# Performance work log

Hardware: AMD Instinct MI355X
Metric: run time of the kernel (lower is better)

The kernel has to match this reference:

```python
import jax, jax.numpy as jnp
import numpy as np

B, T, C, H = 4, 2048, 768, 12
D = C // H  # head_size = 64
ROPE_BASE = 10000.0


def rotary_tables(seq_len, dim, dtype=jnp.float32):
    # dim = head_size; uses dim//2 frequencies
    inv_freq = 1.0 / (ROPE_BASE ** (jnp.arange(0, dim, 2, dtype=jnp.float32) / dim))
    t = jnp.arange(seq_len, dtype=jnp.float32)
    freqs = jnp.outer(t, inv_freq)  # [T, D/2]
    return jnp.cos(freqs).astype(dtype), jnp.sin(freqs).astype(dtype)


def apply_rotary(x, cos, sin):
    # x: [B, H, T, D]; cos/sin: [T, D/2] broadcast over B,H
    d = x.shape[-1] // 2
    x1, x2 = x[..., :d], x[..., d:]
    y1 = x1 * cos + x2 * sin
    y2 = -x1 * sin + x2 * cos
    return jnp.concatenate([y1, y2], axis=-1)


def setup_inputs() -> dict:
    key = jax.random.key(0)
    ks = jax.random.split(key, 5)
    x = jax.random.normal(ks[0], (B, T, C), dtype=jnp.float32)
    W_attn = jax.random.normal(ks[1], (C, 3 * C), dtype=jnp.float32) * (1.0 / np.sqrt(C))
    b_attn = jax.random.normal(ks[2], (3 * C,), dtype=jnp.float32) * 0.02
    W_proj = jax.random.normal(ks[3], (C, C), dtype=jnp.float32) * (1.0 / np.sqrt(C))
    b_proj = jax.random.normal(ks[4], (C,), dtype=jnp.float32) * 0.02
    return {"x": x, "W_attn": W_attn, "b_attn": b_attn, "W_proj": W_proj, "b_proj": b_proj}


def reference(x, W_attn, b_attn, W_proj, b_proj):
    Bx, Tx, Cx = x.shape
    qkv = x @ W_attn + b_attn  # [B, T, 3C]
    q, k, v = jnp.split(qkv, 3, axis=-1)
    # [B, T, C] -> [B, H, T, D]
    to_heads = lambda a: a.reshape(Bx, Tx, H, D).transpose(0, 2, 1, 3)
    q, k, v = to_heads(q), to_heads(k), to_heads(v)
    cos, sin = rotary_tables(Tx, D, x.dtype)
    q = apply_rotary(q, cos, sin)
    k = apply_rotary(k, cos, sin)
    scale = 1.0 / np.sqrt(D)
    scores = jnp.einsum('bhqd,bhkd->bhqk', q, k) * scale  # [B, H, T, T]
    causal = jnp.tril(jnp.ones((Tx, Tx), dtype=bool))
    scores = jnp.where(causal, scores, jnp.finfo(scores.dtype).min)
    attn = jax.nn.softmax(scores, axis=-1)
    y = jnp.einsum('bhqk,bhkd->bhqd', attn, v)  # [B, H, T, D]
    y = y.transpose(0, 2, 1, 3).reshape(Bx, Tx, Cx)
    return y @ W_proj + b_proj
```

## Files before the change

### kernel.cpp

```cpp
#include <hip/hip_runtime.h>
#include <hip/hip_bf16.h>

#define BB 4
#define TT 2048
#define CC 768
#define HH 12
#define DD 64
#define MM (BB * TT)
#define BH (BB * HH)

typedef __bf16 bf16_t;
typedef __bf16 bf16x8 __attribute__((ext_vector_type(8)));
typedef __bf16 bf16x4 __attribute__((ext_vector_type(4)));
typedef float f32x4 __attribute__((ext_vector_type(4)));
typedef float f32x16 __attribute__((ext_vector_type(16)));

__device__ __forceinline__ float fast_exp2(float x) {
#if __has_builtin(__builtin_amdgcn_exp2f)
    return __builtin_amdgcn_exp2f(x);
#else
    return exp2f(x);
#endif
}

__device__ __forceinline__ uint32_t pk2(float lo, float hi) {
    bf16_t l = (bf16_t)lo, h = (bf16_t)hi;
    uint16_t lu = __builtin_bit_cast(uint16_t, l);
    uint16_t hu = __builtin_bit_cast(uint16_t, h);
    return ((uint32_t)hu << 16) | lu;
}

__device__ __forceinline__ void gload_lds16(const void* g, void* l) {
    __builtin_amdgcn_global_load_lds(
        (const __attribute__((address_space(1))) uint32_t*)g,
        (__attribute__((address_space(3))) uint32_t*)l, 16, 0, 0);
}

__global__ void cvt_f32_bf16(const float* __restrict__ in, bf16_t* __restrict__ out, int n4) {
    int tid = blockIdx.x * blockDim.x + threadIdx.x;
    if (tid >= n4) return;
    float4 v = ((const float4*)in)[tid];
    bf16x4 o;
    o[0] = (bf16_t)v.x; o[1] = (bf16_t)v.y; o[2] = (bf16_t)v.z; o[3] = (bf16_t)v.w;
    ((bf16x4*)out)[tid] = o;
}

__global__ void transpose_cvt(const float* __restrict__ W, bf16_t* __restrict__ WT, int K, int N) {
    __shared__ bf16_t tile[32][33];
    int k0 = blockIdx.x * 32, n0 = blockIdx.y * 32;
    int tx = threadIdx.x, ty = threadIdx.y;
#pragma unroll
    for (int r = 0; r < 4; ++r) {
        int kl = ty * 4 + r;
        tile[kl][tx] = (bf16_t)W[(size_t)(k0 + kl) * N + n0 + tx];
    }
    __syncthreads();
#pragma unroll
    for (int r = 0; r < 4; ++r) {
        int nl = ty * 4 + r;
        WT[(size_t)(n0 + nl) * K + k0 + tx] = tile[tx][nl];
    }
}

#define GEMM_CORE(A_, BT_, acc_)                                                       \
    __shared__ bf16_t As[2][128 * 32];                                                 \
    __shared__ bf16_t Bs[2][128 * 32];                                                 \
    int tid = threadIdx.x;                                                             \
    int wv = tid >> 6, lane = tid & 63, c = lane & 15, quad = lane >> 4;               \
    int wm = (wv >> 1) * 64, wn = (wv & 1) * 64;                                       \
    int m0 = blockIdx.x * 128, n0 = blockIdx.y * 128;                                  \
    int srow = wv * 32 + (lane >> 2);                                                  \
    int slot = lane & 3;                                                               \
    auto stage = [&](int buf, int k0) {                                                \
        _Pragma("unroll")                                                              \
        for (int ins = 0; ins < 2; ++ins) {                                            \
            int r = srow + ins * 16;                                                   \
            int g = (slot - ((r >> 1) & 3)) & 3;                                       \
            const bf16_t* ga = A_ + (size_t)(m0 + r) * K + k0 + g * 8;                 \
            const bf16_t* gb = BT_ + (size_t)(n0 + r) * K + k0 + g * 8;                \
            gload_lds16(ga, &As[buf][(wv * 32 + ins * 16) * 32]);                      \
            gload_lds16(gb, &Bs[buf][(wv * 32 + ins * 16) * 32]);                      \
        }                                                                              \
    };                                                                                 \
    int s_rd = (quad + ((c >> 1) & 3)) & 3;                                            \
    const int nk = K / 32;                                                             \
    stage(0, 0);                                                                       \
    for (int kt = 0; kt < nk; ++kt) {                                                  \
        __syncthreads();                                                               \
        if (kt + 1 < nk) stage((kt + 1) & 1, (kt + 1) * 32);                           \
        int buf = kt & 1;                                                              \
        bf16x8 af[4], bfr[4];                                                          \
        _Pragma("unroll")                                                              \
        for (int i = 0; i < 4; ++i) af[i] = *(const bf16x8*)&As[buf][(wm + i * 16 + c) * 32 + s_rd * 8];  \
        _Pragma("unroll")                                                              \
        for (int j = 0; j < 4; ++j) bfr[j] = *(const bf16x8*)&Bs[buf][(wn + j * 16 + c) * 32 + s_rd * 8]; \
        _Pragma("unroll")                                                              \
        for (int i = 0; i < 4; ++i)                                                    \
            _Pragma("unroll")                                                          \
            for (int j = 0; j < 4; ++j)                                                \
                acc_[i][j] = __builtin_amdgcn_mfma_f32_16x16x32_bf16(af[i], bfr[j], acc_[i][j], 0, 0, 0); \
    }

__global__ __launch_bounds__(256, 3) void gemm_qkv(
        const bf16_t* __restrict__ A, const bf16_t* __restrict__ BT,
        const float* __restrict__ bias,
        bf16_t* __restrict__ Qh, bf16_t* __restrict__ Kh, bf16_t* __restrict__ Vt) {
    const int K = 768;
    __shared__ __align__(16) bf16_t smem[17408];
    bf16_t* Asp = smem;
    bf16_t* Bsp = smem + 8192;
    int tid = threadIdx.x;
    int wv = tid >> 6, lane = tid & 63, c = lane & 15, quad = lane >> 4;
    int wm = (wv >> 1) * 64, wn = (wv & 1) * 64;
    int m0 = blockIdx.x * 128, n0 = blockIdx.y * 128;
    int srow = wv * 32 + (lane >> 2);
    int slot = lane & 3;
    auto stage = [&](int buf, int k0) {
#pragma unroll
        for (int ins = 0; ins < 2; ++ins) {
            int r = srow + ins * 16;
            int g = (slot - ((r >> 1) & 3)) & 3;
            gload_lds16(A + (size_t)(m0 + r) * K + k0 + g * 8, &Asp[buf * 4096 + (wv * 32 + ins * 16) * 32]);
            gload_lds16(BT + (size_t)(n0 + r) * K + k0 + g * 8, &Bsp[buf * 4096 + (wv * 32 + ins * 16) * 32]);
        }
    };
    int s_rd = (quad + ((c >> 1) & 3)) & 3;
    f32x4 acc[4][4] = {};
    const int nk = K / 32;
    stage(0, 0);
    for (int kt = 0; kt < nk; ++kt) {
        __syncthreads();
        if (kt + 1 < nk) stage((kt + 1) & 1, (kt + 1) * 32);
        int buf = kt & 1;
        bf16x8 af[4], bfr[4];
#pragma unroll
        for (int i = 0; i < 4; ++i) af[i] = *(const bf16x8*)&Asp[buf * 4096 + (wm + i * 16 + c) * 32 + s_rd * 8];
#pragma unroll
        for (int j = 0; j < 4; ++j) bfr[j] = *(const bf16x8*)&Bsp[buf * 4096 + (wn + j * 16 + c) * 32 + s_rd * 8];
#pragma unroll
        for (int i = 0; i < 4; ++i)
#pragma unroll
            for (int j = 0; j < 4; ++j)
                acc[i][j] = __builtin_amdgcn_mfma_f32_16x16x32_bf16(af[i], bfr[j], acc[i][j], 0, 0, 0);
    }
    __syncthreads();

    int type = n0 / 768;
    int hloc = ((n0 % 768) + wn) >> 6;
    int bidx = m0 >> 11;
    int colb = n0 + wn;
    int tb = (m0 + wm) & (TT - 1);
    bf16_t* epi = smem + wv * 4352;
    int rrow = lane >> 3, cchunk = lane & 7;

    if (type < 2) {
        const float rscale = (type == 0) ? 0.125f * 1.44269504088896f : 1.0f;
#pragma unroll
        for (int j = 0; j < 2; ++j) {
            int dlo = j * 16 + c;
            float infr = fast_exp2(-(float)dlo * 0.4152410118609828f);
            float blo = bias[colb + j * 16 + c];
            float bhi = bias[colb + (j + 2) * 16 + c];
#pragma unroll
            for (int i = 0; i < 4; ++i)
#pragma unroll
                for (int r = 0; r < 4; ++r) {
                    int lr = i * 16 + quad * 4 + r;
                    float a = acc[i][j][r] + blo;
                    float b2 = acc[i][j + 2][r] + bhi;
                    float fr = (float)(tb + lr) * infr;
                    float cs, sn;
                    __sincosf(fr, &sn, &cs);
                    epi[lr * 68 + dlo]      = (bf16_t)((a * cs + b2 * sn) * rscale);
                    epi[lr * 68 + dlo + 32] = (bf16_t)((-a * sn + b2 * cs) * rscale);
                }
        }
        bf16_t* dst = (type == 0 ? Qh : Kh) + (size_t)(bidx * HH + hloc) * TT * DD + (size_t)tb * DD;
#pragma unroll
        for (int it = 0; it < 8; ++it) {
            int row = it * 8 + rrow;
            bf16x8 v = *(const bf16x8*)&epi[row * 68 + cchunk * 8];
            *(bf16x8*)&dst[row * 64 + cchunk * 8] = v;
        }
    } else {
        int kt64 = tb >> 6;
#pragma unroll
        for (int j = 0; j < 4; ++j) {
            int dim = j * 16 + c;
            float bv = bias[colb + j * 16 + c];
            int rot = (dim & 7) * 8;
#pragma unroll
            for (int i = 0; i < 4; ++i)
#pragma unroll
                for (int r = 0; r < 4; ++r) {
                    int tin = i * 16 + quad * 4 + r;
                    epi[dim * 68 + ((tin + rot) & 63)] = (bf16_t)(acc[i][j][r] + bv);
                }
        }
        bf16_t* dstV = Vt + (size_t)(bidx * HH + hloc) * (TT / 64) * 4096 + (size_t)kt64 * 4096;
#pragma unroll
        for (int it = 0; it < 8; ++it) {
            int dim = it * 8 + rrow;
            int src = ((cchunk + (dim & 7)) & 7) * 8;
            bf16x8 v = *(const bf16x8*)&epi[dim * 68 + src];
            *(bf16x8*)&dstV[dim * 64 + cchunk * 8] = v;
        }
    }
}

__global__ __launch_bounds__(256, 3) void gemm_proj(
        const bf16_t* __restrict__ A, const bf16_t* __restrict__ BT,
        const float* __restrict__ bias, float* __restrict__ Cout) {
    const int K = 768;
    f32x4 acc[4][4] = {};
    GEMM_CORE(A, BT, acc)
#pragma unroll
    for (int j = 0; j < 4; ++j) {
        int col = n0 + wn + j * 16 + c;
        float bv = bias[col];
#pragma unroll
        for (int i = 0; i < 4; ++i) {
            int row = m0 + wm + i * 16 + quad * 4;
#pragma unroll
            for (int r = 0; r < 4; ++r)
                Cout[(size_t)(row + r) * CC + col] = acc[i][j][r] + bv;
        }
    }
}

__global__ __launch_bounds__(256, 3) void flash_attn(
        const bf16_t* __restrict__ Q, const bf16_t* __restrict__ Kc,
        const bf16_t* __restrict__ Vt, bf16_t* __restrict__ Y) {
    __shared__ bf16_t Ks[2][64 * 64];
    __shared__ bf16_t Vs[2][64 * 64];
    int blk = blockIdx.x;
    int r0 = (blk < 256) ? blk : ((blk < 512) ? (1023 - blk) : (blk - 256));
    int qt = 15 - (r0 / 48);
    int bh = r0 % 48;
    int wv = threadIdx.x >> 6, lane = threadIdx.x & 63;
    int b = bh / HH, h = bh - b * HH;
    int q31 = lane & 31, hi = lane >> 5;
    int qbw = qt * 128 + wv * 32;
    const bf16_t* Qg = Q + ((size_t)bh * TT + qbw) * DD;
    const bf16_t* Kg = Kc + (size_t)bh * TT * DD;
    const bf16_t* Vg = Vt + (size_t)bh * (TT / 64) * 4096;

    bf16x8 qf[4];
#pragma unroll
    for (int dk = 0; dk < 4; ++dk)
        qf[dk] = *(const bf16x8*)(Qg + (size_t)q31 * DD + dk * 16 + hi * 8);

    int srow = wv * 16 + (lane >> 3);
    int slot = lane & 7;
    auto stage = [&](int buf, int kt64) {
#pragma unroll
        for (int ins = 0; ins < 2; ++ins) {
            int r = srow + ins * 8;
            int g = (slot - (r & 7)) & 7;
            gload_lds16(Kg + (size_t)(kt64 * 64 + r) * 64 + g * 8, &Ks[buf][(wv * 16 + ins * 8) * 64]);
            gload_lds16(Vg + (size_t)kt64 * 4096 + r * 64 + g * 8, &Vs[buf][(wv * 16 + ins * 8) * 64]);
        }
    };

    f32x16 O[2] = {};
    float lsum = 0.0f;

    int ntiles = 2 * qt + 2;
    stage(0, 0);
    for (int kt = 0; kt < ntiles; ++kt) {
        __syncthreads();
        if (kt + 1 < ntiles) stage((kt + 1) & 1, kt + 1);
        int buf = kt & 1;
#pragma unroll
        for (int t32 = 0; t32 < 2; ++t32) {
            int ks = kt * 64 + t32 * 32;
            if (ks > qbw) continue;
            bool masked = (ks == qbw);

            f32x16 st = {};
#pragma unroll
            for (int dk = 0; dk < 4; ++dk) {
                int row = t32 * 32 + q31;
                int sl = ((dk * 2 + hi) + (row & 7)) & 7;
                bf16x8 kf = *(const bf16x8*)&Ks[buf][row * 64 + sl * 8];
                st = __builtin_amdgcn_mfma_f32_32x32x16_bf16(kf, qf[dk], st, 0, 0, 0);
            }

            bf16x8 vf[2][2];
#pragma unroll
            for (int dt = 0; dt < 2; ++dt)
#pragma unroll
                for (int sli = 0; sli < 2; ++sli) {
                    int row = dt * 32 + q31;
                    int ch = t32 * 4 + sli * 2 + hi;
                    int sl = (ch + (row & 7)) & 7;
                    vf[dt][sli] = *(const bf16x8*)&Vs[buf][row * 64 + sl * 8];
                }

            float p[16];
#pragma unroll
            for (int r = 0; r < 16; ++r) {
                float e = fast_exp2(st[r]);
                if (masked) {
                    int keyl = (r & 3) + 8 * (r >> 2) + 4 * hi;
                    if (keyl > q31) e = 0.0f;
                }
                p[r] = e;
            }
            lsum += ((((p[0] + p[1]) + (p[2] + p[3])) + ((p[4] + p[5]) + (p[6] + p[7])))
                  + (((p[8] + p[9]) + (p[10] + p[11])) + ((p[12] + p[13]) + (p[14] + p[15]))));

            union { uint32_t u[4]; bf16x8 v; } pb[2];
#pragma unroll
            for (int sli = 0; sli < 2; ++sli) {
                uint32_t a0 = pk2(p[sli * 8 + 0], p[sli * 8 + 1]);
                uint32_t b0 = pk2(p[sli * 8 + 2], p[sli * 8 + 3]);
                uint32_t a1 = pk2(p[sli * 8 + 4], p[sli * 8 + 5]);
                uint32_t b1 = pk2(p[sli * 8 + 6], p[sli * 8 + 7]);
                asm("v_permlane32_swap_b32 %0, %1" : "+v"(a0), "+v"(a1));
                asm("v_permlane32_swap_b32 %0, %1" : "+v"(b0), "+v"(b1));
                pb[sli].u[0] = a0; pb[sli].u[1] = b0; pb[sli].u[2] = a1; pb[sli].u[3] = b1;
            }

#pragma unroll
            for (int dt = 0; dt < 2; ++dt) {
                O[dt] = __builtin_amdgcn_mfma_f32_32x32x16_bf16(vf[dt][0], pb[0].v, O[dt], 0, 0, 0);
                O[dt] = __builtin_amdgcn_mfma_f32_32x32x16_bf16(vf[dt][1], pb[1].v, O[dt], 0, 0, 0);
            }
        }
    }

    float l = lsum;
    l += __shfl_xor(l, 32);
    float inv_l = 1.0f / l;
    int row = b * TT + qbw + q31;
#pragma unroll
    for (int dt = 0; dt < 2; ++dt)
#pragma unroll
        for (int g = 0; g < 4; ++g) {
            bf16x4 ov;
#pragma unroll
            for (int r = 0; r < 4; ++r) ov[r] = (bf16_t)(O[dt][g * 4 + r] * inv_l);
            *(bf16x4*)(Y + (size_t)row * CC + h * DD + dt * 32 + g * 8 + hi * 4) = ov;
        }
}

extern "C" void kernel_launch(void* const* d_in, const int* in_sizes, int n_in,
                              void* d_out, int out_size, void* d_ws, size_t ws_size,
                              hipStream_t stream) {
    const float* x      = (const float*)d_in[0];
    const float* W_attn = (const float*)d_in[1];
    const float* b_attn = (const float*)d_in[2];
    const float* W_proj = (const float*)d_in[3];
    const float* b_proj = (const float*)d_in[4];
    float* out = (float*)d_out;

    unsigned char* ws = (unsigned char*)d_ws;
    size_t off = 0;
    auto alloc = [&](size_t bytes) { void* p = ws + off; off += (bytes + 255) & ~(size_t)255; return p; };
    bf16_t* xb  = (bf16_t*)alloc((size_t)MM * CC * 2);
    bf16_t* WaT = (bf16_t*)alloc((size_t)3 * CC * CC * 2);
    bf16_t* WpT = (bf16_t*)alloc((size_t)CC * CC * 2);
    bf16_t* Qh  = (bf16_t*)alloc((size_t)BH * TT * DD * 2);
    bf16_t* Kh  = (bf16_t*)alloc((size_t)BH * TT * DD * 2);
    bf16_t* Vt  = (bf16_t*)alloc((size_t)BH * TT * DD * 2);
    bf16_t* Yb  = (bf16_t*)alloc((size_t)MM * CC * 2);

    cvt_f32_bf16<<<(MM * CC / 4 + 255) / 256, 256, 0, stream>>>(x, xb, MM * CC / 4);
    transpose_cvt<<<dim3(CC / 32, 3 * CC / 32), dim3(32, 8), 0, stream>>>(W_attn, WaT, CC, 3 * CC);
    transpose_cvt<<<dim3(CC / 32, CC / 32), dim3(32, 8), 0, stream>>>(W_proj, WpT, CC, CC);
    gemm_qkv<<<dim3(MM / 128, 3 * CC / 128), 256, 0, stream>>>(xb, WaT, b_attn, Qh, Kh, Vt);
    flash_attn<<<dim3(768), 256, 0, stream>>>(Qh, Kh, Vt, Yb);
    gemm_proj<<<dim3(MM / 128, CC / 128), 256, 0, stream>>>(Yb, WpT, b_proj, out);
}
```

Measured before the change: 192.2 us.

## Split long causal query tiles across two blocks and combine partials

The four longest causal query tiles (qt 12-15) are now each split across two blocks along the key dimension. Each half writes unnormalized fp32 O and row sums to a workspace, and a new combine kernel adds them and normalizes. Work is ordered through a constant schedule table to balance load across 960 blocks. The tile loop is also split into unmasked and masked phases, MFMA sections get s_setprio boosts, and LDS is declared as a larger flat buffer. The cost is an extra kernel launch plus the global-memory round trip for the partials. The larger LDS allocation may reduce occupancy.

```diff
diff --git a/kernel.cpp b/kernel.cpp
--- a/kernel.cpp
+++ b/kernel.cpp
@@ -228,15 +228,24 @@
     }
 }
 
+__constant__ signed char RK_QT[20] = {11,10,9,8,15,15,7,14,14,13,13,6,12,12,5,4,3,2,1,0};
+__constant__ signed char RK_PC[20] = { 2, 2,2,2, 0, 1,2, 0, 1, 0, 1,2, 0, 1,2,2,2,2,2,2};
+
 __global__ __launch_bounds__(256, 3) void flash_attn(
         const bf16_t* __restrict__ Q, const bf16_t* __restrict__ Kc,
-        const bf16_t* __restrict__ Vt, bf16_t* __restrict__ Y) {
-    __shared__ bf16_t Ks[2][64 * 64];
-    __shared__ bf16_t Vs[2][64 * 64];
+        const bf16_t* __restrict__ Vt, bf16_t* __restrict__ Y,
+        float* __restrict__ Opart, float* __restrict__ Lpart) {
+    __shared__ __align__(16) bf16_t smem[22016];
+    bf16_t* KsB = smem;
+    bf16_t* VsB = smem + 13824;
+
     int blk = blockIdx.x;
-    int r0 = (blk < 256) ? blk : ((blk < 512) ? (1023 - blk) : (blk - 256));
-    int qt = 15 - (r0 / 48);
-    int bh = r0 % 48;
+    int r = blk / 48, bh = blk - r * 48;
+    int qt = RK_QT[r], pc = RK_PC[r];
+    int kt0 = (pc == 1) ? (qt + 1) : 0;
+    int ktend = (pc == 0) ? (qt + 1) : (2 * qt + 2);
+    int nct = ktend - kt0;
+
     int wv = threadIdx.x >> 6, lane = threadIdx.x & 63;
     int b = bh / HH, h = bh - b * HH;
     int q31 = lane & 31, hi = lane >> 5;
@@ -255,94 +264,147 @@
     auto stage = [&](int buf, int kt64) {
 #pragma unroll
         for (int ins = 0; ins < 2; ++ins) {
-            int r = srow + ins * 8;
-            int g = (slot - (r & 7)) & 7;
-            gload_lds16(Kg + (size_t)(kt64 * 64 + r) * 64 + g * 8, &Ks[buf][(wv * 16 + ins * 8) * 64]);
-            gload_lds16(Vg + (size_t)kt64 * 4096 + r * 64 + g * 8, &Vs[buf][(wv * 16 + ins * 8) * 64]);
+            int rr = srow + ins * 8;
+            int g = (slot - (rr & 7)) & 7;
+            gload_lds16(Kg + (size_t)(kt64 * 64 + rr) * 64 + g * 8, &KsB[buf * 4096 + (wv * 16 + ins * 8) * 64]);
+            gload_lds16(Vg + (size_t)kt64 * 4096 + rr * 64 + g * 8, &VsB[buf * 4096 + (wv * 16 + ins * 8) * 64]);
         }
     };
 
     f32x16 O[2] = {};
     float lsum = 0.0f;
 
-    int ntiles = 2 * qt + 2;
-    stage(0, 0);
-    for (int kt = 0; kt < ntiles; ++kt) {
-        __syncthreads();
-        if (kt + 1 < ntiles) stage((kt + 1) & 1, kt + 1);
-        int buf = kt & 1;
-#pragma unroll
-        for (int t32 = 0; t32 < 2; ++t32) {
-            int ks = kt * 64 + t32 * 32;
-            if (ks > qbw) continue;
-            bool masked = (ks == qbw);
-
-            f32x16 st = {};
-#pragma unroll
-            for (int dk = 0; dk < 4; ++dk) {
-                int row = t32 * 32 + q31;
-                int sl = ((dk * 2 + hi) + (row & 7)) & 7;
-                bf16x8 kf = *(const bf16x8*)&Ks[buf][row * 64 + sl * 8];
-                st = __builtin_amdgcn_mfma_f32_32x32x16_bf16(kf, qf[dk], st, 0, 0, 0);
-            }
-
-            bf16x8 vf[2][2];
-#pragma unroll
-            for (int dt = 0; dt < 2; ++dt)
-#pragma unroll
-                for (int sli = 0; sli < 2; ++sli) {
-                    int row = dt * 32 + q31;
-                    int ch = t32 * 4 + sli * 2 + hi;
-                    int sl = (ch + (row & 7)) & 7;
-                    vf[dt][sli] = *(const bf16x8*)&Vs[buf][row * 64 + sl * 8];
-                }
-
-            float p[16];
-#pragma unroll
-            for (int r = 0; r < 16; ++r) {
-                float e = fast_exp2(st[r]);
-                if (masked) {
-                    int keyl = (r & 3) + 8 * (r >> 2) + 4 * hi;
-                    if (keyl > q31) e = 0.0f;
-                }
-                p[r] = e;
-            }
-            lsum += ((((p[0] + p[1]) + (p[2] + p[3])) + ((p[4] + p[5]) + (p[6] + p[7])))
-                  + (((p[8] + p[9]) + (p[10] + p[11])) + ((p[12] + p[13]) + (p[14] + p[15]))));
-
-            union { uint32_t u[4]; bf16x8 v; } pb[2];
-#pragma unroll
-            for (int sli = 0; sli < 2; ++sli) {
-                uint32_t a0 = pk2(p[sli * 8 + 0], p[sli * 8 + 1]);
-                uint32_t b0 = pk2(p[sli * 8 + 2], p[sli * 8 + 3]);
-                uint32_t a1 = pk2(p[sli * 8 + 4], p[sli * 8 + 5]);
-                uint32_t b1 = pk2(p[sli * 8 + 6], p[sli * 8 + 7]);
-                asm("v_permlane32_swap_b32 %0, %1" : "+v"(a0), "+v"(a1));
-                asm("v_permlane32_swap_b32 %0, %1" : "+v"(b0), "+v"(b1));
-                pb[sli].u[0] = a0; pb[sli].u[1] = b0; pb[sli].u[2] = a1; pb[sli].u[3] = b1;
-            }
-
-#pragma unroll
-            for (int dt = 0; dt < 2; ++dt) {
-                O[dt] = __builtin_amdgcn_mfma_f32_32x32x16_bf16(vf[dt][0], pb[0].v, O[dt], 0, 0, 0);
-                O[dt] = __builtin_amdgcn_mfma_f32_32x32x16_bf16(vf[dt][1], pb[1].v, O[dt], 0, 0, 0);
-            }
-        }
-    }
+    stage(0, kt0);
+
+#define FA_TILE(FULL)                                                                   \
+    {                                                                                   \
+        int kt = kt0 + i;                                                               \
+        int buf = i & 1;                                                                \
+        __syncthreads();                                                                \
+        if (i + 1 < nct) stage((i + 1) & 1, kt + 1);                                    \
+        _Pragma("unroll")                                                               \
+        for (int t32 = 0; t32 < 2; ++t32) {                                             \
+            int ks = kt * 64 + t32 * 32;                                                \
+            if (!(FULL) && ks > qbw) continue;                                          \
+            bool masked = !(FULL) && (ks == qbw);                                       \
+            f32x16 st = {};                                                             \
+            __builtin_amdgcn_s_setprio(1);                                              \
+            _Pragma("unroll")                                                           \
+            for (int dk = 0; dk < 4; ++dk) {                                            \
+                int row = t32 * 32 + q31;                                               \
+                int sl = ((dk * 2 + hi) + (row & 7)) & 7;                               \
+                bf16x8 kf = *(const bf16x8*)&KsB[buf * 4096 + row * 64 + sl * 8];       \
+                st = __builtin_amdgcn_mfma_f32_32x32x16_bf16(kf, qf[dk], st, 0, 0, 0);  \
+            }                                                                           \
+            __builtin_amdgcn_s_setprio(0);                                              \
+            bf16x8 vf[2][2];                                                            \
+            _Pragma("unroll")                                                           \
+            for (int dt = 0; dt < 2; ++dt)                                              \
+                _Pragma("unroll")                                                       \
+                for (int sli = 0; sli < 2; ++sli) {                                     \
+                    int row = dt * 32 + q31;                                            \
+                    int ch = t32 * 4 + sli * 2 + hi;                                    \
+                    int sl = (ch + (row & 7)) & 7;                                      \
+                    vf[dt][sli] = *(const bf16x8*)&VsB[buf * 4096 + row * 64 + sl * 8]; \
+                }                                                                       \
+            float p[16];                                                                \
+            _Pragma("unroll")                                                           \
+            for (int rr = 0; rr < 16; ++rr) {                                           \
+                float e = fast_exp2(st[rr]);                                            \
+                if (masked) {                                                           \
+                    int keyl = (rr & 3) + 8 * (rr >> 2) + 4 * hi;                       \
+                    if (keyl > q31) e = 0.0f;                                           \
+                }                                                                       \
+                p[rr] = e;                                                              \
+            }                                                                           \
+            lsum += ((((p[0] + p[1]) + (p[2] + p[3])) + ((p[4] + p[5]) + (p[6] + p[7])))\
+                  + (((p[8] + p[9]) + (p[10] + p[11])) + ((p[12] + p[13]) + (p[14] + p[15])))); \
+            union { uint32_t u[4]; bf16x8 v; } pb[2];                                   \
+            _Pragma("unroll")                                                           \
+            for (int sli = 0; sli < 2; ++sli) {                                         \
+                uint32_t a0 = pk2(p[sli * 8 + 0], p[sli * 8 + 1]);                      \
+                uint32_t b0 = pk2(p[sli * 8 + 2], p[sli * 8 + 3]);                      \
+                uint32_t a1 = pk2(p[sli * 8 + 4], p[sli * 8 + 5]);                      \
+                uint32_t b1 = pk2(p[sli * 8 + 6], p[sli * 8 + 7]);                      \
+                asm("v_permlane32_swap_b32 %0, %1" : "+v"(a0), "+v"(a1));               \
+                asm("v_permlane32_swap_b32 %0, %1" : "+v"(b0), "+v"(b1));               \
+                pb[sli].u[0] = a0; pb[sli].u[1] = b0; pb[sli].u[2] = a1; pb[sli].u[3] = b1; \
+            }                                                                           \
+            __builtin_amdgcn_s_setprio(1);                                              \
+            _Pragma("unroll")                                                           \
+            for (int dt = 0; dt < 2; ++dt) {                                            \
+                O[dt] = __builtin_amdgcn_mfma_f32_32x32x16_bf16(vf[dt][0], pb[0].v, O[dt], 0, 0, 0); \
+                O[dt] = __builtin_amdgcn_mfma_f32_32x32x16_bf16(vf[dt][1], pb[1].v, O[dt], 0, 0, 0); \
+            }                                                                           \
+            __builtin_amdgcn_s_setprio(0);                                              \
+        }                                                                               \
+    }
+
+    int nfull = 2 * qt - kt0;
+    if (nfull > nct) nfull = nct;
+    if (nfull < 0) nfull = 0;
+    int i = 0;
+    for (; i < nfull; ++i) FA_TILE(1)
+    for (; i < nct; ++i) FA_TILE(0)
+#undef FA_TILE
 
     float l = lsum;
     l += __shfl_xor(l, 32);
-    float inv_l = 1.0f / l;
-    int row = b * TT + qbw + q31;
-#pragma unroll
-    for (int dt = 0; dt < 2; ++dt)
-#pragma unroll
-        for (int g = 0; g < 4; ++g) {
-            bf16x4 ov;
-#pragma unroll
-            for (int r = 0; r < 4; ++r) ov[r] = (bf16_t)(O[dt][g * 4 + r] * inv_l);
-            *(bf16x4*)(Y + (size_t)row * CC + h * DD + dt * 32 + g * 8 + hi * 4) = ov;
-        }
+
+    if (pc == 2) {
+        float inv_l = 1.0f / l;
+        int row = b * TT + qbw + q31;
+#pragma unroll
+        for (int dt = 0; dt < 2; ++dt)
+#pragma unroll
+            for (int g = 0; g < 4; ++g) {
+                bf16x4 ov;
+#pragma unroll
+                for (int rr = 0; rr < 4; ++rr) ov[rr] = (bf16_t)(O[dt][g * 4 + rr] * inv_l);
+                *(bf16x4*)(Y + (size_t)row * CC + h * DD + dt * 32 + g * 8 + hi * 4) = ov;
+            }
+    } else {
+        int pslot = bh * 4 + (qt - 12);
+        int idx = pslot * 2 + pc;
+        float* Op = Opart + ((size_t)idx * 128 + wv * 32 + q31) * 64;
+#pragma unroll
+        for (int dt = 0; dt < 2; ++dt)
+#pragma unroll
+            for (int g = 0; g < 4; ++g) {
+                f32x4 ov;
+#pragma unroll
+                for (int rr = 0; rr < 4; ++rr) ov[rr] = O[dt][g * 4 + rr];
+                *(f32x4*)(Op + dt * 32 + g * 8 + hi * 4) = ov;
+            }
+        if (hi == 0) Lpart[idx * 128 + wv * 32 + q31] = l;
+    }
+}
+
+__global__ __launch_bounds__(256, 4) void combine_partials(
+        const float* __restrict__ Opart, const float* __restrict__ Lpart,
+        bf16_t* __restrict__ Y) {
+    int pslot = blockIdx.x;
+    int bh = pslot >> 2, qt = 12 + (pslot & 3);
+    int b = bh / HH, h = bh - b * HH;
+    int t = threadIdx.x;
+    int q = t >> 1, dh = (t & 1) * 32;
+    const float* p0 = Opart + ((size_t)(pslot * 2 + 0) * 128 + q) * 64 + dh;
+    const float* p1 = Opart + ((size_t)(pslot * 2 + 1) * 128 + q) * 64 + dh;
+    float inv = 1.0f / (Lpart[(pslot * 2 + 0) * 128 + q] + Lpart[(pslot * 2 + 1) * 128 + q]);
+    bf16_t* y = Y + ((size_t)(b * TT + qt * 128 + q)) * CC + h * DD + dh;
+#pragma unroll
+    for (int g = 0; g < 4; ++g) {
+        f32x4 a = *(const f32x4*)(p0 + g * 8);
+        f32x4 a2 = *(const f32x4*)(p0 + g * 8 + 4);
+        f32x4 c = *(const f32x4*)(p1 + g * 8);
+        f32x4 c2 = *(const f32x4*)(p1 + g * 8 + 4);
+        bf16x8 o;
+#pragma unroll
+        for (int rr = 0; rr < 4; ++rr) o[rr] = (bf16_t)((a[rr] + c[rr]) * inv);
+#pragma unroll
+        for (int rr = 0; rr < 4; ++rr) o[4 + rr] = (bf16_t)((a2[rr] + c2[rr]) * inv);
+        *(bf16x8*)(y + g * 8) = o;
+    }
 }
 
 extern "C" void kernel_launch(void* const* d_in, const int* in_sizes, int n_in,
@@ -365,11 +427,14 @@
     bf16_t* Kh  = (bf16_t*)alloc((size_t)BH * TT * DD * 2);
     bf16_t* Vt  = (bf16_t*)alloc((size_t)BH * TT * DD * 2);
     bf16_t* Yb  = (bf16_t*)alloc((size_t)MM * CC * 2);
+    float*  Opart = (float*)alloc((size_t)192 * 2 * 128 * 64 * 4);
+    float*  Lpart = (float*)alloc((size_t)192 * 2 * 128 * 4);
 
     cvt_f32_bf16<<<(MM * CC / 4 + 255) / 256, 256, 0, stream>>>(x, xb, MM * CC / 4);
     transpose_cvt<<<dim3(CC / 32, 3 * CC / 32), dim3(32, 8), 0, stream>>>(W_attn, WaT, CC, 3 * CC);
     transpose_cvt<<<dim3(CC / 32, CC / 32), dim3(32, 8), 0, stream>>>(W_proj, WpT, CC, CC);
     gemm_qkv<<<dim3(MM / 128, 3 * CC / 128), 256, 0, stream>>>(xb, WaT, b_attn, Qh, Kh, Vt);
-    flash_attn<<<dim3(768), 256, 0, stream>>>(Qh, Kh, Vt, Yb);
+    flash_attn<<<dim3(960), 256, 0, stream>>>(Qh, Kh, Vt, Yb, Opart, Lpart);
+    combine_partials<<<dim3(192), 256, 0, stream>>>(Opart, Lpart, Yb);
     gemm_proj<<<dim3(MM / 128, CC / 128), 256, 0, stream>>>(Yb, WpT, b_proj, out);
 }
```

Measured after the change: 187.7 us. 1.02x faster.
